# Kernel optimization log

Measured on AMD Instinct MI355X. Metric: run time of the kernel, lower is better.

## Reference

```python
import jax, jax.numpy as jnp
import numpy as np

C_M, C_Z, C, H = 256, 128, 32, 8
N_SEQ, N_RES = 256, 256
EPS = 1e-5


def _layer_norm(x, w, b):
    mu = jnp.mean(x, axis=-1, keepdims=True)
    var = jnp.mean(jnp.square(x - mu), axis=-1, keepdims=True)
    return (x - mu) * jax.lax.rsqrt(var + EPS) * w + b


def setup_inputs() -> dict:
    key = jax.random.key(0)
    ks = jax.random.split(key, 10)
    s = lambda fan_in: 1.0 / np.sqrt(fan_in)
    return {
        "m": jax.random.normal(ks[0], (N_SEQ, N_RES, C_M), jnp.float32),
        "z": jax.random.normal(ks[1], (N_RES, N_RES, C_Z), jnp.float32),
        "ln_m_w": jnp.ones((C_M,), jnp.float32),
        "ln_m_b": jnp.zeros((C_M,), jnp.float32),
        "ln_z_w": jnp.ones((C_Z,), jnp.float32),
        "ln_z_b": jnp.zeros((C_Z,), jnp.float32),
        "w_z": jax.random.normal(ks[2], (C_Z, H), jnp.float32) * s(C_Z),
        "w_q": jax.random.normal(ks[3], (C_M, H * C), jnp.float32) * s(C_M),
        "w_k": jax.random.normal(ks[4], (C_M, H * C), jnp.float32) * s(C_M),
        "w_v": jax.random.normal(ks[5], (C_M, H * C), jnp.float32) * s(C_M),
        "w_g": jax.random.normal(ks[6], (C_M, H * C), jnp.float32) * s(C_M),
        "b_g": jnp.zeros((H * C,), jnp.float32),
        "w_o": jax.random.normal(ks[7], (H * C, C_M), jnp.float32) * s(H * C),
        "b_o": jnp.zeros((C_M,), jnp.float32),
    }


def reference(m, z, ln_m_w, ln_m_b, ln_z_w, ln_z_b, w_z, w_q, w_k, w_v, w_g, b_g, w_o, b_o):
    S, R = m.shape[0], m.shape[1]
    mn = _layer_norm(m, ln_m_w, ln_m_b)                      # (S, R, c_m)
    # pair bias: LN + Linear(c_z -> H), then movedim(-1, -3): (R, R, H) -> (H, R, R)
    bias = jnp.moveaxis(_layer_norm(z, ln_z_w, ln_z_b) @ w_z, -1, -3)

    q = (mn @ w_q).reshape(S, R, H, C)
    k = (mn @ w_k).reshape(S, R, H, C)
    v = (mn @ w_v).reshape(S, R, H, C)

    scale = 1.0 / np.sqrt(C)
    # attention over residue axis (attn_dim=-2); bias broadcast over N_seq
    logits = jnp.einsum("sqhd,skhd->shqk", q, k) * scale + bias[None]  # (S, H, R, R)
    attn = jax.nn.softmax(logits, axis=-1)
    o = jnp.einsum("shqk,skhd->sqhd", attn, v).reshape(S, R, H * C)

    g = jax.nn.sigmoid(mn @ w_g + b_g)                       # (S, R, H*c)
    return (g * o) @ w_o + b_o                               # (S, R, c_m)
```

## Files before the change

kernel.cpp:

```cpp
#include <hip/hip_runtime.h>
#include <hip/hip_bf16.h>

typedef __hip_bfloat16 bf16;
typedef __attribute__((ext_vector_type(8))) short short8;
typedef __attribute__((ext_vector_type(16))) float f32x16;

#define NS 256
#define NR 256
#define CM 256
#define CZ 128
#define NH 8
#define CH 32
#define LN_EPS 1e-5f
#define LOG2E 1.4426950408889634f
#define SCALE2 (0.17677669529663687f * 1.4426950408889634f)

__device__ __forceinline__ unsigned pk_bf16(float lo, float hi) {
  unsigned r;
  asm volatile("v_cvt_pk_bf16_f32 %0, %1, %2" : "=v"(r) : "v"(lo), "v"(hi));
  return r;
}

__device__ __forceinline__ short8 load8(const bf16* p) {
  return __builtin_bit_cast(short8, *(const uint4*)p);
}

__global__ __launch_bounds__(256) void pack_w_kernel(
    const float* __restrict__ wq, const float* __restrict__ wk,
    const float* __restrict__ wv, const float* __restrict__ wg,
    const float* __restrict__ wo, bf16* __restrict__ dst) {
  int mat = blockIdx.y;
  const float* src = mat == 0 ? wq : mat == 1 ? wk : mat == 2 ? wv
                   : mat == 3 ? wg : wo;
  float sc = (mat == 0) ? SCALE2 : 1.0f;
  int t = blockIdx.x * 256 + threadIdx.x;
  int n = t & 255;
  int hi = (t >> 8) & 1;
  int kc = t >> 9;
  int kbase = kc * 16 + hi * 8;
  bf16 tmp[8];
  #pragma unroll
  for (int j = 0; j < 8; ++j)
    tmp[j] = __float2bfloat16(src[(size_t)(kbase + j) * 256 + n] * sc);
  *(uint4*)(dst + (size_t)mat * 65536 +
            ((size_t)(kc * 2 + hi) * 256 + n) * 8) = *(const uint4*)tmp;
}

__global__ __launch_bounds__(256) void ln_m_kernel(
    const float* __restrict__ m, const float* __restrict__ w,
    const float* __restrict__ b, bf16* __restrict__ mn) {
  int row = blockIdx.x * 4 + (threadIdx.x >> 6);
  int lane = threadIdx.x & 63;

  float4 x = ((const float4*)(m + (size_t)row * CM))[lane];
  float sum = x.x + x.y + x.z + x.w;
  #pragma unroll
  for (int off = 32; off; off >>= 1) sum += __shfl_xor(sum, off);
  float mu = sum * (1.0f / CM);

  float dx = x.x - mu, dy = x.y - mu, dz = x.z - mu, dw = x.w - mu;
  float ss = dx * dx + dy * dy + dz * dz + dw * dw;
  #pragma unroll
  for (int off = 32; off; off >>= 1) ss += __shfl_xor(ss, off);
  float rs = rsqrtf(ss * (1.0f / CM) + LN_EPS);

  float4 wv = ((const float4*)w)[lane];
  float4 bv = ((const float4*)b)[lane];
  unsigned p0 = pk_bf16(dx * rs * wv.x + bv.x, dy * rs * wv.y + bv.y);
  unsigned p1 = pk_bf16(dz * rs * wv.z + bv.z, dw * rs * wv.w + bv.w);
  uint2 u;
  u.x = p0;
  u.y = p1;
  *(uint2*)(mn + (size_t)row * CM + lane * 4) = u;
}

__global__ __launch_bounds__(128) void bias_kernel(
    const float* __restrict__ z, const float* __restrict__ w,
    const float* __restrict__ b, const float* __restrict__ wz,
    float* __restrict__ biasP) {
  int row = blockIdx.x;
  int t = threadIdx.x;
  __shared__ float red[2];
  __shared__ float zn[CZ];
  __shared__ float part[16][9];

  float x = z[(size_t)row * CZ + t];

  float v = x;
  #pragma unroll
  for (int off = 32; off; off >>= 1) v += __shfl_xor(v, off);
  if ((t & 63) == 0) red[t >> 6] = v;
  __syncthreads();
  float mu = (red[0] + red[1]) * (1.0f / CZ);
  float d = x - mu;
  __syncthreads();

  v = d * d;
  #pragma unroll
  for (int off = 32; off; off >>= 1) v += __shfl_xor(v, off);
  if ((t & 63) == 0) red[t >> 6] = v;
  __syncthreads();
  float var = (red[0] + red[1]) * (1.0f / CZ);

  zn[t] = d * rsqrtf(var + LN_EPS) * w[t] + b[t];
  __syncthreads();

  int h = t & 7, grp = t >> 3;
  float acc = 0.0f;
  #pragma unroll
  for (int cc = 0; cc < 8; ++cc) {
    int c = grp * 8 + cc;
    acc += zn[c] * wz[c * NH + h];
  }
  part[grp][h] = acc;
  __syncthreads();

  if (t < NH) {
    float s = 0.0f;
    #pragma unroll
    for (int g = 0; g < 16; ++g) s += part[g][t];
    int i = row >> 8, j = row & 255;
    int qt = i >> 5, lo = i & 31;
    int tt = j >> 5, rem = j & 31;
    int hi2 = (rem >> 2) & 1;
    int r = ((rem >> 3) << 2) | (rem & 3);
    int ifrag = tt * 16 + r;
    int lane = hi2 * 32 + lo;
    biasP[((((size_t)t * 8 + qt) * 32 + (ifrag >> 2)) * 64 + lane) * 4 +
          (ifrag & 3)] = s * LOG2E;
  }
}

__global__ __launch_bounds__(256, 2) void qkvg_mfma_kernel(
    const bf16* __restrict__ mn, const bf16* __restrict__ wp,
    const float* __restrict__ bg,
    bf16* __restrict__ qo, bf16* __restrict__ ko,
    bf16* __restrict__ vo, bf16* __restrict__ go) {
  int mat = threadIdx.x >> 6;
  int lane = threadIdx.x & 63;
  int lo = lane & 31, hi = lane >> 5;
  size_t m0 = (size_t)blockIdx.x * 32;

  const bf16* arow = mn + (m0 + lo) * 256 + hi * 8;
  const bf16* wbase = wp + (size_t)mat * 65536 + ((size_t)hi * 256 + lo) * 8;

  f32x16 acc[8] = {};
  #pragma unroll 2
  for (int kc = 0; kc < 16; ++kc) {
    short8 a = load8(arow + kc * 16);
    const bf16* wkc = wbase + (size_t)kc * 4096;
    #pragma unroll
    for (int nt = 0; nt < 8; ++nt) {
      short8 b = load8(wkc + nt * 256);
      acc[nt] = __builtin_amdgcn_mfma_f32_32x32x16_bf16(a, b, acc[nt], 0, 0, 0);
    }
  }

  bf16* outp = mat == 0 ? qo : mat == 1 ? ko : mat == 2 ? vo : go;
  if (mat == 3) {
    #pragma unroll
    for (int nt = 0; nt < 8; ++nt) {
      float bgv = bg[nt * 32 + lo];
      #pragma unroll
      for (int r = 0; r < 16; ++r) {
        int crow = (r & 3) + ((r >> 2) << 3) + (hi << 2);
        float sv = 1.0f / (1.0f + __expf(-(acc[nt][r] + bgv)));
        outp[(m0 + crow) * 256 + nt * 32 + lo] = __float2bfloat16(sv);
      }
    }
  } else {
    #pragma unroll
    for (int nt = 0; nt < 8; ++nt) {
      #pragma unroll
      for (int r = 0; r < 16; ++r) {
        int crow = (r & 3) + ((r >> 2) << 3) + (hi << 2);
        outp[(m0 + crow) * 256 + nt * 32 + lo] = __float2bfloat16(acc[nt][r]);
      }
    }
  }
}

__global__ __launch_bounds__(256) void transpose_v_kernel(
    const bf16* __restrict__ vo, bf16* __restrict__ vT) {
  int s = blockIdx.x >> 3, h = blockIdx.x & 7;
  int t = threadIdx.x;
  __shared__ bf16 tile[256][40];

  #pragma unroll
  for (int p = 0; p < 4; ++p) {
    int k = p * 64 + (t >> 2);
    int c0 = (t & 3) * 8;
    uint4 u = *(const uint4*)(vo + ((size_t)(s * 256 + k)) * 256 + h * 32 + c0);
    *(uint4*)&tile[k][c0] = u;
  }
  __syncthreads();

  int c = t >> 3, k0 = (t & 7) * 32;
  bf16 buf[32];
  #pragma unroll
  for (int j = 0; j < 32; ++j) buf[j] = tile[k0 + j][c];
  bf16* dst = vT + (((size_t)(s * 8 + h) * 32 + c) * 256 + k0);
  #pragma unroll
  for (int q = 0; q < 4; ++q)
    *(uint4*)(dst + q * 8) = *(const uint4*)(buf + q * 8);
}

__global__ __launch_bounds__(256, 3) void attn_mfma_kernel(
    const bf16* __restrict__ qb, const bf16* __restrict__ kb,
    const bf16* __restrict__ vT, const bf16* __restrict__ gb,
    const float* __restrict__ biasP, bf16* __restrict__ gob) {
  int wb = (blockIdx.x & 7) * 512 + (blockIdx.x >> 3);
  int wid = wb * 4 + (threadIdx.x >> 6);
  int lane = threadIdx.x & 63;
  int lo = lane & 31;
  int hi = lane >> 5;
  int s = wid >> 6;
  int h = (wid >> 3) & 7;
  int qt = wid & 7;
  int q0 = qt * 32;

  const size_t base = (size_t)s * NR * 256 + h * CH;

  const float4* bp4 =
      (const float4*)biasP + ((size_t)(h * 8 + qt) * 32) * 64 + lane;

  short8 qf[2];
  #pragma unroll
  for (int cc = 0; cc < 2; ++cc)
    qf[cc] = load8(qb + base + (size_t)(q0 + lo) * 256 + cc * 16 + hi * 8);

  const bf16* vt = vT + ((size_t)(s * NH + h) * CH + lo) * 256;

  f32x16 o = {};
  float l0 = 0.0f, l1 = 0.0f, l2 = 0.0f, l3 = 0.0f;

  #pragma unroll
  for (int hs = 0; hs < 2; ++hs) {
    f32x16 acc[4];
    __builtin_amdgcn_s_setprio(1);
    #pragma unroll
    for (int th = 0; th < 4; ++th) {
      int t = hs * 4 + th;
      short8 kf0 = load8(kb + base + (size_t)(t * 32 + lo) * 256 + hi * 8);
      short8 kf1 = load8(kb + base + (size_t)(t * 32 + lo) * 256 + 16 + hi * 8);
      f32x16 z = {};
      acc[th] = __builtin_amdgcn_mfma_f32_32x32x16_bf16(kf0, qf[0], z, 0, 0, 0);
      acc[th] =
          __builtin_amdgcn_mfma_f32_32x32x16_bf16(kf1, qf[1], acc[th], 0, 0, 0);
    }
    __builtin_amdgcn_s_setprio(0);

    #pragma unroll
    for (int th = 0; th < 4; ++th) {
      int t = hs * 4 + th;
      #pragma unroll
      for (int j = 0; j < 4; ++j) {
        float4 b4 = bp4[(t * 4 + j) * 64];
        float e0 = exp2f(acc[th][j * 4 + 0] + b4.x);
        float e1 = exp2f(acc[th][j * 4 + 1] + b4.y);
        float e2 = exp2f(acc[th][j * 4 + 2] + b4.z);
        float e3 = exp2f(acc[th][j * 4 + 3] + b4.w);
        acc[th][j * 4 + 0] = e0;
        acc[th][j * 4 + 1] = e1;
        acc[th][j * 4 + 2] = e2;
        acc[th][j * 4 + 3] = e3;
        l0 += e0;
        l1 += e1;
        l2 += e2;
        l3 += e3;
      }
    }

    #pragma unroll
    for (int kc2 = 0; kc2 < 8; ++kc2) {
      int th = kc2 >> 1;
      int rb = (kc2 & 1) << 3;
      unsigned uL0 = pk_bf16(acc[th][rb + 0], acc[th][rb + 1]);
      unsigned uL1 = pk_bf16(acc[th][rb + 2], acc[th][rb + 3]);
      unsigned uH0 = pk_bf16(acc[th][rb + 4], acc[th][rb + 5]);
      unsigned uH1 = pk_bf16(acc[th][rb + 6], acc[th][rb + 7]);
      unsigned sL0 = __shfl_xor(uL0, 32), sL1 = __shfl_xor(uL1, 32);
      unsigned sH0 = __shfl_xor(uH0, 32), sH1 = __shfl_xor(uH1, 32);
      uint4 pu;
      pu.x = hi ? sH0 : uL0;
      pu.y = hi ? sH1 : uL1;
      pu.z = hi ? uH0 : sL0;
      pu.w = hi ? uH1 : sL1;
      short8 pf = __builtin_bit_cast(short8, pu);
      short8 vf = load8(vt + (hs * 8 + kc2) * 16 + hi * 8);
      o = __builtin_amdgcn_mfma_f32_32x32x16_bf16(pf, vf, o, 0, 0, 0);
    }
  }

  float l = (l0 + l1) + (l2 + l3);
  l += __shfl_xor(l, 32);
  float linv = 1.0f / l;

  #pragma unroll
  for (int r = 0; r < 16; ++r) {
    int crow = (r & 3) + ((r >> 2) << 3) + (hi << 2);
    float li = __shfl(linv, crow);
    size_t idx = base + (size_t)(q0 + crow) * 256 + lo;
    float gg = __bfloat162float(gb[idx]);
    gob[idx] = __float2bfloat16(gg * o[r] * li);
  }
}

__global__ __launch_bounds__(256, 2) void out_mfma_kernel(
    const bf16* __restrict__ gob, const bf16* __restrict__ wop,
    const float* __restrict__ bo, float* __restrict__ out) {
  int wid = blockIdx.x * 4 + (threadIdx.x >> 6);
  int lane = threadIdx.x & 63;
  int lo = lane & 31, hi = lane >> 5;
  size_t m0 = (size_t)wid * 32;

  const bf16* arow = gob + (m0 + lo) * 256 + hi * 8;
  const bf16* wbase = wop + ((size_t)hi * 256 + lo) * 8;

  f32x16 acc[8] = {};
  #pragma unroll 2
  for (int kc = 0; kc < 16; ++kc) {
    short8 a = load8(arow + kc * 16);
    const bf16* wkc = wbase + (size_t)kc * 4096;
    #pragma unroll
    for (int nt = 0; nt < 8; ++nt) {
      short8 b = load8(wkc + nt * 256);
      acc[nt] = __builtin_amdgcn_mfma_f32_32x32x16_bf16(a, b, acc[nt], 0, 0, 0);
    }
  }

  #pragma unroll
  for (int nt = 0; nt < 8; ++nt) {
    float bv = bo[nt * 32 + lo];
    #pragma unroll
    for (int r = 0; r < 16; ++r) {
      int crow = (r & 3) + ((r >> 2) << 3) + (hi << 2);
      out[(m0 + crow) * 256 + nt * 32 + lo] = acc[nt][r] + bv;
    }
  }
}

extern "C" void kernel_launch(void* const* d_in, const int* in_sizes, int n_in,
                              void* d_out, int out_size, void* d_ws, size_t ws_size,
                              hipStream_t stream) {
  const float* m      = (const float*)d_in[0];
  const float* z      = (const float*)d_in[1];
  const float* ln_m_w = (const float*)d_in[2];
  const float* ln_m_b = (const float*)d_in[3];
  const float* ln_z_w = (const float*)d_in[4];
  const float* ln_z_b = (const float*)d_in[5];
  const float* w_z    = (const float*)d_in[6];
  const float* w_q    = (const float*)d_in[7];
  const float* w_k    = (const float*)d_in[8];
  const float* w_v    = (const float*)d_in[9];
  const float* w_g    = (const float*)d_in[10];
  const float* b_g    = (const float*)d_in[11];
  const float* w_o    = (const float*)d_in[12];
  const float* b_o    = (const float*)d_in[13];
  float* out = (float*)d_out;

  const size_t SZ = (size_t)NS * NR * 256;

  bf16* mn   = (bf16*)d_ws;
  bf16* qb   = mn + SZ;
  bf16* kb   = qb + SZ;
  bf16* vo   = kb + SZ;
  bf16* gb   = vo + SZ;
  bf16* gob  = gb + SZ;
  float* biasP = (float*)(gob + SZ);
  bf16* wp   = (bf16*)(biasP + NH * NR * NR);
  bf16* wop  = wp + 4 * 65536;
  bf16* vT   = mn;

  pack_w_kernel<<<dim3(32, 5), 256, 0, stream>>>(w_q, w_k, w_v, w_g, w_o, wp);
  ln_m_kernel<<<(NS * NR) / 4, 256, 0, stream>>>(m, ln_m_w, ln_m_b, mn);
  bias_kernel<<<NR * NR, 128, 0, stream>>>(z, ln_z_w, ln_z_b, w_z, biasP);
  qkvg_mfma_kernel<<<(NS * NR) / 32, 256, 0, stream>>>(mn, wp, b_g,
                                                       qb, kb, vo, gb);
  transpose_v_kernel<<<NS * NH, 256, 0, stream>>>(vo, vT);
  attn_mfma_kernel<<<(NS * NH * 8) / 4, 256, 0, stream>>>(qb, kb, vT, gb,
                                                          biasP, gob);
  out_mfma_kernel<<<(NS * NR) / 32 / 4, 256, 0, stream>>>(gob, wop, b_o, out);
}
```

Baseline: 299.3 us.

## Fuse msa layernorm into QKVG projection, batch bias rows, split output GEMM

Removes the separate layernorm kernel over m. The QKVG kernel now loads fp32 m directly, computes mean and variance from one-pass sum and sum of squares, and normalizes in registers before the MFMA loop. This avoids writing and re-reading the bf16 normalized tensor. The cost is that each of the four matrix waves in a block recomputes the same layernorm, and the raw values are rounded to bf16 before normalization, which adds error. The pair-bias kernel now handles two rows per 256-thread block, and the output GEMM is split into two halves with a higher occupancy hint.

```diff
diff --git a/kernel.cpp b/kernel.cpp
--- a/kernel.cpp
+++ b/kernel.cpp
@@ -46,79 +46,52 @@
             ((size_t)(kc * 2 + hi) * 256 + n) * 8) = *(const uint4*)tmp;
 }
 
-__global__ __launch_bounds__(256) void ln_m_kernel(
-    const float* __restrict__ m, const float* __restrict__ w,
-    const float* __restrict__ b, bf16* __restrict__ mn) {
-  int row = blockIdx.x * 4 + (threadIdx.x >> 6);
-  int lane = threadIdx.x & 63;
-
-  float4 x = ((const float4*)(m + (size_t)row * CM))[lane];
-  float sum = x.x + x.y + x.z + x.w;
-  #pragma unroll
-  for (int off = 32; off; off >>= 1) sum += __shfl_xor(sum, off);
-  float mu = sum * (1.0f / CM);
-
-  float dx = x.x - mu, dy = x.y - mu, dz = x.z - mu, dw = x.w - mu;
-  float ss = dx * dx + dy * dy + dz * dz + dw * dw;
-  #pragma unroll
-  for (int off = 32; off; off >>= 1) ss += __shfl_xor(ss, off);
-  float rs = rsqrtf(ss * (1.0f / CM) + LN_EPS);
-
-  float4 wv = ((const float4*)w)[lane];
-  float4 bv = ((const float4*)b)[lane];
-  unsigned p0 = pk_bf16(dx * rs * wv.x + bv.x, dy * rs * wv.y + bv.y);
-  unsigned p1 = pk_bf16(dz * rs * wv.z + bv.z, dw * rs * wv.w + bv.w);
-  uint2 u;
-  u.x = p0;
-  u.y = p1;
-  *(uint2*)(mn + (size_t)row * CM + lane * 4) = u;
-}
-
-__global__ __launch_bounds__(128) void bias_kernel(
+__global__ __launch_bounds__(256) void bias_kernel(
     const float* __restrict__ z, const float* __restrict__ w,
     const float* __restrict__ b, const float* __restrict__ wz,
     float* __restrict__ biasP) {
-  int row = blockIdx.x;
-  int t = threadIdx.x;
-  __shared__ float red[2];
-  __shared__ float zn[CZ];
-  __shared__ float part[16][9];
-
-  float x = z[(size_t)row * CZ + t];
+  int rh = threadIdx.x >> 7;
+  int tr = threadIdx.x & 127;
+  int row = blockIdx.x * 2 + rh;
+  __shared__ float red[2][2];
+  __shared__ float zn[2][CZ];
+  __shared__ float part[2][16][9];
+
+  float x = z[(size_t)row * CZ + tr];
 
   float v = x;
   #pragma unroll
   for (int off = 32; off; off >>= 1) v += __shfl_xor(v, off);
-  if ((t & 63) == 0) red[t >> 6] = v;
-  __syncthreads();
-  float mu = (red[0] + red[1]) * (1.0f / CZ);
+  if ((tr & 63) == 0) red[rh][tr >> 6] = v;
+  __syncthreads();
+  float mu = (red[rh][0] + red[rh][1]) * (1.0f / CZ);
   float d = x - mu;
   __syncthreads();
 
   v = d * d;
   #pragma unroll
   for (int off = 32; off; off >>= 1) v += __shfl_xor(v, off);
-  if ((t & 63) == 0) red[t >> 6] = v;
-  __syncthreads();
-  float var = (red[0] + red[1]) * (1.0f / CZ);
-
-  zn[t] = d * rsqrtf(var + LN_EPS) * w[t] + b[t];
-  __syncthreads();
-
-  int h = t & 7, grp = t >> 3;
+  if ((tr & 63) == 0) red[rh][tr >> 6] = v;
+  __syncthreads();
+  float var = (red[rh][0] + red[rh][1]) * (1.0f / CZ);
+
+  zn[rh][tr] = d * rsqrtf(var + LN_EPS) * w[tr] + b[tr];
+  __syncthreads();
+
+  int h = tr & 7, grp = tr >> 3;
   float acc = 0.0f;
   #pragma unroll
   for (int cc = 0; cc < 8; ++cc) {
     int c = grp * 8 + cc;
-    acc += zn[c] * wz[c * NH + h];
-  }
-  part[grp][h] = acc;
-  __syncthreads();
-
-  if (t < NH) {
+    acc += zn[rh][c] * wz[c * NH + h];
+  }
+  part[rh][grp][h] = acc;
+  __syncthreads();
+
+  if (tr < NH) {
     float s = 0.0f;
     #pragma unroll
-    for (int g = 0; g < 16; ++g) s += part[g][t];
+    for (int g = 0; g < 16; ++g) s += part[rh][g][tr];
     int i = row >> 8, j = row & 255;
     int qt = i >> 5, lo = i & 31;
     int tt = j >> 5, rem = j & 31;
@@ -126,13 +99,14 @@
     int r = ((rem >> 3) << 2) | (rem & 3);
     int ifrag = tt * 16 + r;
     int lane = hi2 * 32 + lo;
-    biasP[((((size_t)t * 8 + qt) * 32 + (ifrag >> 2)) * 64 + lane) * 4 +
+    biasP[((((size_t)tr * 8 + qt) * 32 + (ifrag >> 2)) * 64 + lane) * 4 +
           (ifrag & 3)] = s * LOG2E;
   }
 }
 
 __global__ __launch_bounds__(256, 2) void qkvg_mfma_kernel(
-    const bf16* __restrict__ mn, const bf16* __restrict__ wp,
+    const float* __restrict__ m, const float* __restrict__ lnw,
+    const float* __restrict__ lnb, const bf16* __restrict__ wp,
     const float* __restrict__ bg,
     bf16* __restrict__ qo, bf16* __restrict__ ko,
     bf16* __restrict__ vo, bf16* __restrict__ go) {
@@ -141,13 +115,74 @@
   int lo = lane & 31, hi = lane >> 5;
   size_t m0 = (size_t)blockIdx.x * 32;
 
-  const bf16* arow = mn + (m0 + lo) * 256 + hi * 8;
+  const float* mrow = m + (m0 + lo) * 256 + hi * 8;
+
+  short8 af[16];
+  float sum = 0.0f, ssq = 0.0f;
+  #pragma unroll
+  for (int kc = 0; kc < 16; ++kc) {
+    float4 x0 = *(const float4*)(mrow + kc * 16);
+    float4 x1 = *(const float4*)(mrow + kc * 16 + 4);
+    sum += (x0.x + x0.y) + (x0.z + x0.w) + (x1.x + x1.y) + (x1.z + x1.w);
+    ssq = fmaf(x0.x, x0.x, ssq);
+    ssq = fmaf(x0.y, x0.y, ssq);
+    ssq = fmaf(x0.z, x0.z, ssq);
+    ssq = fmaf(x0.w, x0.w, ssq);
+    ssq = fmaf(x1.x, x1.x, ssq);
+    ssq = fmaf(x1.y, x1.y, ssq);
+    ssq = fmaf(x1.z, x1.z, ssq);
+    ssq = fmaf(x1.w, x1.w, ssq);
+    uint4 u;
+    u.x = pk_bf16(x0.x, x0.y);
+    u.y = pk_bf16(x0.z, x0.w);
+    u.z = pk_bf16(x1.x, x1.y);
+    u.w = pk_bf16(x1.z, x1.w);
+    af[kc] = __builtin_bit_cast(short8, u);
+  }
+  sum += __shfl_xor(sum, 32);
+  ssq += __shfl_xor(ssq, 32);
+  float mu = sum * (1.0f / CM);
+  float var = ssq * (1.0f / CM) - mu * mu;
+  float rs = rsqrtf(var + LN_EPS);
+
+  const float* wrow = lnw + hi * 8;
+  const float* brow = lnb + hi * 8;
+  #pragma unroll
+  for (int kc = 0; kc < 16; ++kc) {
+    uint4 u = __builtin_bit_cast(uint4, af[kc]);
+    float4 w0 = *(const float4*)(wrow + kc * 16);
+    float4 w1 = *(const float4*)(wrow + kc * 16 + 4);
+    float4 b0 = *(const float4*)(brow + kc * 16);
+    float4 b1 = *(const float4*)(brow + kc * 16 + 4);
+    float e0 = __uint_as_float(u.x << 16);
+    float e1 = __uint_as_float(u.x & 0xffff0000u);
+    float e2 = __uint_as_float(u.y << 16);
+    float e3 = __uint_as_float(u.y & 0xffff0000u);
+    float e4 = __uint_as_float(u.z << 16);
+    float e5 = __uint_as_float(u.z & 0xffff0000u);
+    float e6 = __uint_as_float(u.w << 16);
+    float e7 = __uint_as_float(u.w & 0xffff0000u);
+    e0 = fmaf((e0 - mu) * rs, w0.x, b0.x);
+    e1 = fmaf((e1 - mu) * rs, w0.y, b0.y);
+    e2 = fmaf((e2 - mu) * rs, w0.z, b0.z);
+    e3 = fmaf((e3 - mu) * rs, w0.w, b0.w);
+    e4 = fmaf((e4 - mu) * rs, w1.x, b1.x);
+    e5 = fmaf((e5 - mu) * rs, w1.y, b1.y);
+    e6 = fmaf((e6 - mu) * rs, w1.z, b1.z);
+    e7 = fmaf((e7 - mu) * rs, w1.w, b1.w);
+    u.x = pk_bf16(e0, e1);
+    u.y = pk_bf16(e2, e3);
+    u.z = pk_bf16(e4, e5);
+    u.w = pk_bf16(e6, e7);
+    af[kc] = __builtin_bit_cast(short8, u);
+  }
+
   const bf16* wbase = wp + (size_t)mat * 65536 + ((size_t)hi * 256 + lo) * 8;
 
   f32x16 acc[8] = {};
   #pragma unroll 2
   for (int kc = 0; kc < 16; ++kc) {
-    short8 a = load8(arow + kc * 16);
+    short8 a = af[kc];
     const bf16* wkc = wbase + (size_t)kc * 4096;
     #pragma unroll
     for (int nt = 0; nt < 8; ++nt) {
@@ -306,7 +341,7 @@
   }
 }
 
-__global__ __launch_bounds__(256, 2) void out_mfma_kernel(
+__global__ __launch_bounds__(256, 3) void out_mfma_kernel(
     const bf16* __restrict__ gob, const bf16* __restrict__ wop,
     const float* __restrict__ bo, float* __restrict__ out) {
   int wid = blockIdx.x * 4 + (threadIdx.x >> 6);
@@ -317,25 +352,30 @@
   const bf16* arow = gob + (m0 + lo) * 256 + hi * 8;
   const bf16* wbase = wop + ((size_t)hi * 256 + lo) * 8;
 
-  f32x16 acc[8] = {};
-  #pragma unroll 2
-  for (int kc = 0; kc < 16; ++kc) {
-    short8 a = load8(arow + kc * 16);
-    const bf16* wkc = wbase + (size_t)kc * 4096;
-    #pragma unroll
-    for (int nt = 0; nt < 8; ++nt) {
-      short8 b = load8(wkc + nt * 256);
-      acc[nt] = __builtin_amdgcn_mfma_f32_32x32x16_bf16(a, b, acc[nt], 0, 0, 0);
-    }
-  }
-
-  #pragma unroll
-  for (int nt = 0; nt < 8; ++nt) {
-    float bv = bo[nt * 32 + lo];
-    #pragma unroll
-    for (int r = 0; r < 16; ++r) {
-      int crow = (r & 3) + ((r >> 2) << 3) + (hi << 2);
-      out[(m0 + crow) * 256 + nt * 32 + lo] = acc[nt][r] + bv;
+  #pragma unroll
+  for (int half = 0; half < 2; ++half) {
+    f32x16 acc[4] = {};
+    #pragma unroll 4
+    for (int kc = 0; kc < 16; ++kc) {
+      short8 a = load8(arow + kc * 16);
+      const bf16* wkc = wbase + (size_t)kc * 4096;
+      #pragma unroll
+      for (int ntl = 0; ntl < 4; ++ntl) {
+        int nt = half * 4 + ntl;
+        short8 b = load8(wkc + nt * 256);
+        acc[ntl] =
+            __builtin_amdgcn_mfma_f32_32x32x16_bf16(a, b, acc[ntl], 0, 0, 0);
+      }
+    }
+    #pragma unroll
+    for (int ntl = 0; ntl < 4; ++ntl) {
+      int nt = half * 4 + ntl;
+      float bv = bo[nt * 32 + lo];
+      #pragma unroll
+      for (int r = 0; r < 16; ++r) {
+        int crow = (r & 3) + ((r >> 2) << 3) + (hi << 2);
+        out[(m0 + crow) * 256 + nt * 32 + lo] = acc[ntl][r] + bv;
+      }
     }
   }
 }
@@ -361,8 +401,8 @@
 
   const size_t SZ = (size_t)NS * NR * 256;
 
-  bf16* mn   = (bf16*)d_ws;
-  bf16* qb   = mn + SZ;
+  bf16* vT   = (bf16*)d_ws;
+  bf16* qb   = vT + SZ;
   bf16* kb   = qb + SZ;
   bf16* vo   = kb + SZ;
   bf16* gb   = vo + SZ;
@@ -370,13 +410,11 @@
   float* biasP = (float*)(gob + SZ);
   bf16* wp   = (bf16*)(biasP + NH * NR * NR);
   bf16* wop  = wp + 4 * 65536;
-  bf16* vT   = mn;
 
   pack_w_kernel<<<dim3(32, 5), 256, 0, stream>>>(w_q, w_k, w_v, w_g, w_o, wp);
-  ln_m_kernel<<<(NS * NR) / 4, 256, 0, stream>>>(m, ln_m_w, ln_m_b, mn);
-  bias_kernel<<<NR * NR, 128, 0, stream>>>(z, ln_z_w, ln_z_b, w_z, biasP);
-  qkvg_mfma_kernel<<<(NS * NR) / 32, 256, 0, stream>>>(mn, wp, b_g,
-                                                       qb, kb, vo, gb);
+  bias_kernel<<<(NR * NR) / 2, 256, 0, stream>>>(z, ln_z_w, ln_z_b, w_z, biasP);
+  qkvg_mfma_kernel<<<(NS * NR) / 32, 256, 0, stream>>>(
+      m, ln_m_w, ln_m_b, wp, b_g, qb, kb, vo, gb);
   transpose_v_kernel<<<NS * NH, 256, 0, stream>>>(vo, vT);
   attn_mfma_kernel<<<(NS * NH * 8) / 4, 256, 0, stream>>>(qb, kb, vT, gb,
                                                           biasP, gob);
```

Measured after the change: 397.0 us. 32.7% more time.
